# Performance work log

Hardware: AMD Instinct MI355X
Metric: run time of the kernel (lower is better)

Reference implementation:

```python
import jax, jax.numpy as jnp
import numpy as np

B, H, KVH, D = 64, 32, 8, 128     # batch, q heads, kv heads, head dim
BS, MB = 16, 128                  # paged-cache block size, max blocks per seq
NB = B * MB                       # total cache blocks (8192)
L = MB * BS                       # max kv length per sequence (2048)
SCALE = 0.08838834764831845       # 1/sqrt(head_dim)


def setup_inputs() -> dict:
    key = jax.random.key(0)
    ks = jax.random.split(key, 6)
    q = jax.random.normal(ks[0], (B, H * D), jnp.float32)
    k = jax.random.normal(ks[1], (B, KVH * D), jnp.float32)
    v = jax.random.normal(ks[2], (B, KVH * D), jnp.float32)
    k_cache = jax.random.normal(ks[3], (NB, BS, KVH, D), jnp.float32)
    v_cache = jax.random.normal(ks[4], (NB, BS, KVH, D), jnp.float32)
    # each sequence owns MB disjoint contiguous blocks
    block_tables = jnp.arange(B * MB, dtype=jnp.int32).reshape(B, MB)
    context_lens = jax.random.randint(ks[5], (B,), 0, L - 1, dtype=jnp.int32)
    return dict(q=q, k=k, v=v, k_cache=k_cache, v_cache=v_cache,
                block_tables=block_tables, context_lens=context_lens)


def reference(q, k, v, k_cache, v_cache, block_tables, context_lens):
    G = H // KVH  # GQA group size
    qh = q.reshape(B, KVH, G, D)
    kh = k.reshape(B, KVH, D)
    vh = v.reshape(B, KVH, D)
    # store new token's KV at its paged slot (position = context_len)
    slots = block_tables[jnp.arange(B), context_lens // BS] * BS + context_lens % BS
    kc = k_cache.reshape(NB * BS, KVH, D).at[slots].set(kh)
    vc = v_cache.reshape(NB * BS, KVH, D).at[slots].set(vh)
    # gather paged KV per sequence via block tables -> [B, L, KVH, D]
    keys = kc.reshape(NB, BS, KVH, D)[block_tables].reshape(B, L, KVH, D)
    vals = vc.reshape(NB, BS, KVH, D)[block_tables].reshape(B, L, KVH, D)
    # GQA attention: each kv head serves G query heads
    scores = jnp.einsum('bkgd,blkd->bkgl', qh, keys) * SCALE
    valid = jnp.arange(L)[None, :] <= context_lens[:, None]  # [B, L], inclusive of new token
    scores = jnp.where(valid[:, None, None, :], scores, jnp.float32(-jnp.inf))
    w = jax.nn.softmax(scores, axis=-1)
    out = jnp.einsum('bkgl,blkd->bkgd', w, vals)
    return out.reshape(B, H * D)
```

## Files before the change

kernel.cpp:

```cpp
#include <hip/hip_runtime.h>
#include <hip/hip_fp16.h>

#define BATCH 64
#define NHEADS 32
#define KVH 8
#define HDIM 128
#define GQA 4
#define BLKSZ 16
#define MAXBLK 128
#define MAXLEN 2048
#define SCALE 0.08838834764831845f

#define CHUNK 64
#define MAXITEMS 2048
#define REC_BYTES 320u
#define SLOT_BYTES 4096u
#define WS_REC_FLOATS ((size_t)MAXITEMS * KVH * GQA * (REC_BYTES / 4))
#define WS_FLOATS (WS_REC_FLOATS + 80)

typedef unsigned int uint;
typedef float f32x4 __attribute__((ext_vector_type(4)));

struct KVBuf { float4 k0, k1, v0, v1; };

template<int CTRL>
__device__ __forceinline__ float dppAdd(float x) {
    int y = __builtin_amdgcn_update_dpp(0, __float_as_int(x), CTRL, 0xf, 0xf, false);
    return x + __int_as_float(y);
}

__device__ __forceinline__ float halfSum(float v, bool upper) {
    v = dppAdd<0x111>(v);
    v = dppAdd<0x112>(v);
    v = dppAdd<0x114>(v);
    v = dppAdd<0x118>(v);
    v = dppAdd<0x142>(v);
    const float lo = __int_as_float(__builtin_amdgcn_readlane(__float_as_int(v), 31));
    const float hi = __int_as_float(__builtin_amdgcn_readlane(__float_as_int(v), 63));
    return upper ? hi : lo;
}

__global__ void pa_scan(const int* __restrict__ context_lens, uint* __restrict__ offs) {
    const int t = threadIdx.x;
    int cnt = (t < BATCH) ? (context_lens[t] + 1 + CHUNK - 1) / CHUNK : 0;
    #pragma unroll
    for (int o = 1; o < 64; o <<= 1) {
        const int v = __shfl_up(cnt, o, 64);
        if (t >= o) cnt += v;
    }
    offs[t + 1] = (uint)cnt;
    if (t == 0) offs[0] = 0u;
}

__global__ __launch_bounds__(256, 4) void pa_partial(
    const float* __restrict__ q,
    const float* __restrict__ knew,
    const float* __restrict__ vnew,
    const float* __restrict__ k_cache,
    const float* __restrict__ v_cache,
    const int*   __restrict__ block_tables,
    const int*   __restrict__ context_lens,
    float* __restrict__ ws,
    const uint*  __restrict__ offs)
{
    const uint item = blockIdx.x;
    if (item >= offs[BATCH]) return;

    int lo = 0, hi = BATCH;
    while (lo + 1 < hi) {
        const int mid = (lo + hi) >> 1;
        if (item >= offs[mid]) lo = mid; else hi = mid;
    }
    const int b    = lo;
    const int part = (int)(item - offs[b]);

    const int cl = context_lens[b];
    const int n  = cl + 1;
    const int p0 = part * CHUNK;
    const int pend = min(p0 + CHUNK, n);

    const int tid  = threadIdx.x;
    const int kvh  = tid >> 5;
    const int lane = tid & 31;
    const bool upperHalf = (tid & 32) != 0;
    const uint laneByte = ((uint)kvh << 9) + ((uint)lane << 4);

    float4 qf[GQA];
    #pragma unroll
    for (int g = 0; g < GQA; ++g) {
        float4 t = *reinterpret_cast<const float4*>(
            &q[(size_t)b * (NHEADS * HDIM) + (size_t)(kvh * GQA + g) * HDIM + lane * 4]);
        t.x *= SCALE; t.y *= SCALE; t.z *= SCALE; t.w *= SCALE;
        qf[g] = t;
    }

    float  s[GQA];
    float4 acc[GQA];
    #pragma unroll
    for (int g = 0; g < GQA; ++g) {
        s[g] = 0.f;
        acc[g] = make_float4(0.f, 0.f, 0.f, 0.f);
    }

    const char* kc8 = reinterpret_cast<const char*>(k_cache);
    const char* vc8 = reinterpret_cast<const char*>(v_cache);

    if (p0 + CHUNK <= cl) {
        int blkv[4];
        #pragma unroll
        for (int c = 0; c < 4; ++c)
            blkv[c] = block_tables[b * MAXBLK + (p0 >> 4) + c];

        KVBuf bufA, bufB;

#define ISSUE(P, i)                                                              \
        {                                                                        \
            const uint u0 = ((uint)blkv[(2*(i)) >> 4] * BLKSZ + ((2*(i)) & 15)) * SLOT_BYTES + laneByte; \
            const uint u1 = ((uint)blkv[(2*(i)+1) >> 4] * BLKSZ + ((2*(i)+1) & 15)) * SLOT_BYTES + laneByte; \
            buf##P.k0 = *reinterpret_cast<const float4*>(kc8 + u0);              \
            buf##P.k1 = *reinterpret_cast<const float4*>(kc8 + u1);              \
            buf##P.v0 = *reinterpret_cast<const float4*>(vc8 + u0);              \
            buf##P.v1 = *reinterpret_cast<const float4*>(vc8 + u1);              \
        }

#define CONSUME(P)                                                               \
        {                                                                        \
            float sc0[GQA], sc1[GQA];                                            \
            _Pragma("unroll")                                                    \
            for (int g = 0; g < GQA; ++g) {                                      \
                sc0[g] = buf##P.k0.x * qf[g].x + buf##P.k0.y * qf[g].y           \
                       + buf##P.k0.z * qf[g].z + buf##P.k0.w * qf[g].w;          \
                sc1[g] = buf##P.k1.x * qf[g].x + buf##P.k1.y * qf[g].y           \
                       + buf##P.k1.z * qf[g].z + buf##P.k1.w * qf[g].w;          \
            }                                                                    \
            _Pragma("unroll")                                                    \
            for (int g = 0; g < GQA; ++g) {                                      \
                sc0[g] = halfSum(sc0[g], upperHalf);                             \
                sc1[g] = halfSum(sc1[g], upperHalf);                             \
            }                                                                    \
            _Pragma("unroll")                                                    \
            for (int g = 0; g < GQA; ++g) {                                      \
                const float e0 = __expf(sc0[g]);                                 \
                const float e1 = __expf(sc1[g]);                                 \
                s[g] += e0 + e1;                                                 \
                acc[g].x += e0 * buf##P.v0.x + e1 * buf##P.v1.x;                 \
                acc[g].y += e0 * buf##P.v0.y + e1 * buf##P.v1.y;                 \
                acc[g].z += e0 * buf##P.v0.z + e1 * buf##P.v1.z;                 \
                acc[g].w += e0 * buf##P.v0.w + e1 * buf##P.v1.w;                 \
            }                                                                    \
        }

        ISSUE(A, 0);
        #pragma unroll
        for (int i = 0; i < 31; ++i) {
            if (i & 1) { ISSUE(A, i + 1); CONSUME(B); }
            else       { ISSUE(B, i + 1); CONSUME(A); }
        }
        CONSUME(B);
#undef ISSUE
#undef CONSUME
    } else {
        const int* bt = &block_tables[b * MAXBLK];
        const float* knrow = &knew[((size_t)b * KVH + kvh) * HDIM + lane * 4];
        const float* vnrow = &vnew[((size_t)b * KVH + kvh) * HDIM + lane * 4];

        for (int t0 = p0; t0 < pend; t0 += 4) {
            bool valid[4];
            const float* kp[4];
            const float* vp[4];
            #pragma unroll
            for (int j = 0; j < 4; ++j) {
                const int l = t0 + j;
                valid[j] = (l < pend);
                if (!valid[j] || l == cl) {
                    kp[j] = knrow; vp[j] = vnrow;
                } else {
                    const int blk = bt[l >> 4];
                    const uint u  = ((uint)blk * BLKSZ + (l & 15)) * SLOT_BYTES + laneByte;
                    kp[j] = reinterpret_cast<const float*>(kc8 + u);
                    vp[j] = reinterpret_cast<const float*>(vc8 + u);
                }
            }

            float4 kf[4], vf[4];
            #pragma unroll
            for (int j = 0; j < 4; ++j) kf[j] = *reinterpret_cast<const float4*>(kp[j]);
            #pragma unroll
            for (int j = 0; j < 4; ++j) vf[j] = *reinterpret_cast<const float4*>(vp[j]);

            float sc[4][GQA];
            #pragma unroll
            for (int j = 0; j < 4; ++j)
                #pragma unroll
                for (int g = 0; g < GQA; ++g)
                    sc[j][g] = kf[j].x * qf[g].x + kf[j].y * qf[g].y
                             + kf[j].z * qf[g].z + kf[j].w * qf[g].w;

            #pragma unroll
            for (int off = 16; off > 0; off >>= 1)
                #pragma unroll
                for (int j = 0; j < 4; ++j)
                    #pragma unroll
                    for (int g = 0; g < GQA; ++g)
                        sc[j][g] += __shfl_xor(sc[j][g], off, 32);

            #pragma unroll
            for (int g = 0; g < GQA; ++g) {
                float p[4];
                #pragma unroll
                for (int j = 0; j < 4; ++j)
                    p[j] = valid[j] ? __expf(sc[j][g]) : 0.f;
                s[g] += (p[0] + p[1]) + (p[2] + p[3]);
                acc[g].x += p[0] * vf[0].x + p[1] * vf[1].x + p[2] * vf[2].x + p[3] * vf[3].x;
                acc[g].y += p[0] * vf[0].y + p[1] * vf[1].y + p[2] * vf[2].y + p[3] * vf[3].y;
                acc[g].z += p[0] * vf[0].z + p[1] * vf[1].z + p[2] * vf[2].z + p[3] * vf[3].z;
                acc[g].w += p[0] * vf[0].w + p[1] * vf[1].w + p[2] * vf[2].w + p[3] * vf[3].w;
            }
        }
    }

    char* rec = reinterpret_cast<char*>(ws)
              + (size_t)(item * KVH + kvh) * GQA * REC_BYTES;
    #pragma unroll
    for (int g = 0; g < GQA; ++g) {
        __half2 h01 = __floats2half2_rn(acc[g].x, acc[g].y);
        __half2 h23 = __floats2half2_rn(acc[g].z, acc[g].w);
        uint2 pk;
        pk.x = *reinterpret_cast<uint*>(&h01);
        pk.y = *reinterpret_cast<uint*>(&h23);
        *reinterpret_cast<uint2*>(rec + (size_t)g * REC_BYTES + lane * 8) = pk;
    }
    if (lane == 0) {
        #pragma unroll
        for (int g = 0; g < GQA; ++g)
            *reinterpret_cast<float*>(rec + (size_t)g * REC_BYTES + 256) = s[g];
    }
}

__global__ __launch_bounds__(128) void pa_reduce(
    const float* __restrict__ ws,
    const uint*  __restrict__ offs,
    float* __restrict__ out)
{
    const int bh   = blockIdx.x;
    const int b    = bh >> 3;
    const int kvh  = bh & 7;
    const int t    = threadIdx.x;
    const int g    = t >> 5;
    const int lane = t & 31;

    const uint i0   = offs[b];
    const int  pcnt = (int)(offs[b + 1] - i0);

    const char* base = reinterpret_cast<const char*>(ws)
                     + ((size_t)(i0 * KVH + kvh) * GQA + g) * REC_BYTES;
    const size_t pstride = (size_t)KVH * GQA * REC_BYTES;

    f32x4 O0 = {0,0,0,0}, O1 = {0,0,0,0}, O2 = {0,0,0,0}, O3 = {0,0,0,0};
    float S0 = 0.f, S1 = 0.f, S2 = 0.f, S3 = 0.f;

#define ACCREC(Ov, Sv, rp)                                                       \
    {                                                                            \
        const uint2 pk = *reinterpret_cast<const uint2*>((rp) + lane * 8);       \
        const float2 f01 = __half22float2(*reinterpret_cast<const __half2*>(&pk.x)); \
        const float2 f23 = __half22float2(*reinterpret_cast<const __half2*>(&pk.y)); \
        Ov.x += f01.x; Ov.y += f01.y; Ov.z += f23.x; Ov.w += f23.y;              \
        Sv += *reinterpret_cast<const float*>((rp) + 256);                       \
    }

    int p = 0;
    for (; p + 4 <= pcnt; p += 4) {
        const char* r0 = base + (size_t)(p + 0) * pstride;
        const char* r1 = base + (size_t)(p + 1) * pstride;
        const char* r2 = base + (size_t)(p + 2) * pstride;
        const char* r3 = base + (size_t)(p + 3) * pstride;
        ACCREC(O0, S0, r0);
        ACCREC(O1, S1, r1);
        ACCREC(O2, S2, r2);
        ACCREC(O3, S3, r3);
    }
    for (; p < pcnt; ++p) {
        const char* r = base + (size_t)p * pstride;
        ACCREC(O0, S0, r);
    }
#undef ACCREC

    const f32x4 O = (O0 + O1) + (O2 + O3);
    const float S = (S0 + S1) + (S2 + S3);
    const float inv = 1.0f / S;

    float* op = &out[(size_t)b * (NHEADS * HDIM) + (size_t)(kvh * GQA + g) * HDIM + lane * 4];
    *reinterpret_cast<f32x4*>(op) = O * inv;
}

__global__ __launch_bounds__(256) void paged_attn_decode(
    const float* __restrict__ q,
    const float* __restrict__ knew,
    const float* __restrict__ vnew,
    const float* __restrict__ k_cache,
    const float* __restrict__ v_cache,
    const int*   __restrict__ block_tables,
    const int*   __restrict__ context_lens,
    float* __restrict__ out)
{
    const int bh   = blockIdx.x;
    const int b    = bh / KVH;
    const int kvh  = bh % KVH;
    const int tid  = threadIdx.x;
    const int hw   = tid >> 5;
    const int lane = tid & 31;

    const int cl = context_lens[b];
    const int n  = cl + 1;

    float4 qf[GQA];
    #pragma unroll
    for (int g = 0; g < GQA; ++g) {
        float4 t = *reinterpret_cast<const float4*>(
            &q[(size_t)b * (NHEADS * HDIM) + (size_t)(kvh * GQA + g) * HDIM + lane * 4]);
        t.x *= SCALE; t.y *= SCALE; t.z *= SCALE; t.w *= SCALE;
        qf[g] = t;
    }

    float  s[GQA];
    float4 acc[GQA];
    #pragma unroll
    for (int g = 0; g < GQA; ++g) { s[g] = 0.f; acc[g] = make_float4(0.f,0.f,0.f,0.f); }

    const int* bt = &block_tables[b * MAXBLK];

    for (int l = hw; l < n; l += 8) {
        const float4* krow;
        const float4* vrow;
        if (l == cl) {
            krow = reinterpret_cast<const float4*>(&knew[(size_t)(b * KVH + kvh) * HDIM]);
            vrow = reinterpret_cast<const float4*>(&vnew[(size_t)(b * KVH + kvh) * HDIM]);
        } else {
            const int    blk = bt[l >> 4];
            const size_t off = (((size_t)blk * BLKSZ + (l & 15)) * KVH + kvh) * HDIM;
            krow = reinterpret_cast<const float4*>(&k_cache[off]);
            vrow = reinterpret_cast<const float4*>(&v_cache[off]);
        }
        const float4 kf = krow[lane];
        const float4 vf = vrow[lane];

        float sc[GQA];
        #pragma unroll
        for (int g = 0; g < GQA; ++g)
            sc[g] = kf.x * qf[g].x + kf.y * qf[g].y + kf.z * qf[g].z + kf.w * qf[g].w;

        #pragma unroll
        for (int off = 16; off > 0; off >>= 1)
            #pragma unroll
            for (int g = 0; g < GQA; ++g)
                sc[g] += __shfl_xor(sc[g], off, 32);

        #pragma unroll
        for (int g = 0; g < GQA; ++g) {
            const float p = __expf(sc[g]);
            s[g] += p;
            acc[g].x += p * vf.x; acc[g].y += p * vf.y;
            acc[g].z += p * vf.z; acc[g].w += p * vf.w;
        }
    }

    __shared__ float lds_s[8][GQA];
    __shared__ float lds_acc[8][GQA][HDIM];

    #pragma unroll
    for (int g = 0; g < GQA; ++g)
        *reinterpret_cast<float4*>(&lds_acc[hw][g][lane * 4]) = acc[g];
    if (lane == 0) {
        #pragma unroll
        for (int g = 0; g < GQA; ++g) lds_s[hw][g] = s[g];
    }
    __syncthreads();

    for (int i = tid; i < GQA * HDIM; i += 256) {
        const int g = i >> 7;
        const int d = i & 127;
        float S = 0.f, O = 0.f;
        #pragma unroll
        for (int h = 0; h < 8; ++h) { S += lds_s[h][g]; O += lds_acc[h][g][d]; }
        out[(size_t)b * (NHEADS * HDIM) + (size_t)(kvh * GQA + g) * HDIM + d] = O / S;
    }
}

extern "C" void kernel_launch(void* const* d_in, const int* in_sizes, int n_in,
                              void* d_out, int out_size, void* d_ws, size_t ws_size,
                              hipStream_t stream) {
    const float* q      = (const float*)d_in[0];
    const float* k      = (const float*)d_in[1];
    const float* v      = (const float*)d_in[2];
    const float* kc     = (const float*)d_in[3];
    const float* vc     = (const float*)d_in[4];
    const int*   bt     = (const int*)d_in[5];
    const int*   clens  = (const int*)d_in[6];
    float*       out    = (float*)d_out;

    if (ws_size >= WS_FLOATS * sizeof(float)) {
        float* ws   = (float*)d_ws;
        uint*  offs = (uint*)(ws + WS_REC_FLOATS);
        pa_scan<<<dim3(1), dim3(64), 0, stream>>>(clens, offs);
        pa_partial<<<dim3(MAXITEMS), dim3(256), 0, stream>>>(
            q, k, v, kc, vc, bt, clens, ws, offs);
        pa_reduce<<<dim3(BATCH * KVH), dim3(128), 0, stream>>>(ws, offs, out);
    } else {
        paged_attn_decode<<<dim3(BATCH * KVH), dim3(256), 0, stream>>>(
            q, k, v, kc, vc, bt, clens, out);
    }
}
```

Measured before the change: 118.3 us.

## Fuse scan, partial and reduce kernels into one with last-block reduction

Every workgroup now computes the chunk prefix offsets itself in shared memory, which removes the separate scan kernel. The last workgroup to finish for a sequence, detected with an atomic counter, performs that sequence's cross-chunk reduction, which removes the separate reduce kernel. Three launches become one memset plus one kernel. The trade-offs are a redundant scan in every block, threadfences and atomics, and a serial tail where a single block reduces all 8 heads of a sequence.

```diff
diff --git a/kernel.cpp b/kernel.cpp
--- a/kernel.cpp
+++ b/kernel.cpp
@@ -16,7 +16,7 @@
 #define REC_BYTES 320u
 #define SLOT_BYTES 4096u
 #define WS_REC_FLOATS ((size_t)MAXITEMS * KVH * GQA * (REC_BYTES / 4))
-#define WS_FLOATS (WS_REC_FLOATS + 80)
+#define WS_FLOATS (WS_REC_FLOATS + 64)
 
 typedef unsigned int uint;
 typedef float f32x4 __attribute__((ext_vector_type(4)));
@@ -40,19 +40,7 @@
     return upper ? hi : lo;
 }
 
-__global__ void pa_scan(const int* __restrict__ context_lens, uint* __restrict__ offs) {
-    const int t = threadIdx.x;
-    int cnt = (t < BATCH) ? (context_lens[t] + 1 + CHUNK - 1) / CHUNK : 0;
-    #pragma unroll
-    for (int o = 1; o < 64; o <<= 1) {
-        const int v = __shfl_up(cnt, o, 64);
-        if (t >= o) cnt += v;
-    }
-    offs[t + 1] = (uint)cnt;
-    if (t == 0) offs[0] = 0u;
-}
-
-__global__ __launch_bounds__(256, 4) void pa_partial(
+__global__ __launch_bounds__(256, 4) void pa_fused(
     const float* __restrict__ q,
     const float* __restrict__ knew,
     const float* __restrict__ vnew,
@@ -61,25 +49,44 @@
     const int*   __restrict__ block_tables,
     const int*   __restrict__ context_lens,
     float* __restrict__ ws,
-    const uint*  __restrict__ offs)
+    uint*  __restrict__ ctr,
+    float* __restrict__ out)
 {
+    __shared__ uint s_offs[BATCH + 1];
+    __shared__ int  s_last;
+
+    const int tid = threadIdx.x;
+
+    if (tid < 64) {
+        int cnt = (tid < BATCH) ? (context_lens[tid] + 1 + CHUNK - 1) / CHUNK : 0;
+        #pragma unroll
+        for (int o = 1; o < 64; o <<= 1) {
+            const int v = __shfl_up(cnt, o, 64);
+            if (tid >= o) cnt += v;
+        }
+        s_offs[tid + 1] = (uint)cnt;
+        if (tid == 0) s_offs[0] = 0u;
+    }
+    __syncthreads();
+
     const uint item = blockIdx.x;
-    if (item >= offs[BATCH]) return;
+    if (item >= s_offs[BATCH]) return;
 
     int lo = 0, hi = BATCH;
     while (lo + 1 < hi) {
         const int mid = (lo + hi) >> 1;
-        if (item >= offs[mid]) lo = mid; else hi = mid;
+        if (item >= s_offs[mid]) lo = mid; else hi = mid;
     }
     const int b    = lo;
-    const int part = (int)(item - offs[b]);
+    const int part = (int)(item - s_offs[b]);
+    const uint i0  = s_offs[b];
+    const int pcnt = (int)(s_offs[b + 1] - i0);
 
     const int cl = context_lens[b];
     const int n  = cl + 1;
     const int p0 = part * CHUNK;
     const int pend = min(p0 + CHUNK, n);
 
-    const int tid  = threadIdx.x;
     const int kvh  = tid >> 5;
     const int lane = tid & 31;
     const bool upperHalf = (tid & 32) != 0;
@@ -219,78 +226,72 @@
         }
     }
 
-    char* rec = reinterpret_cast<char*>(ws)
-              + (size_t)(item * KVH + kvh) * GQA * REC_BYTES;
-    #pragma unroll
-    for (int g = 0; g < GQA; ++g) {
-        __half2 h01 = __floats2half2_rn(acc[g].x, acc[g].y);
-        __half2 h23 = __floats2half2_rn(acc[g].z, acc[g].w);
-        uint2 pk;
-        pk.x = *reinterpret_cast<uint*>(&h01);
-        pk.y = *reinterpret_cast<uint*>(&h23);
-        *reinterpret_cast<uint2*>(rec + (size_t)g * REC_BYTES + lane * 8) = pk;
-    }
-    if (lane == 0) {
-        #pragma unroll
-        for (int g = 0; g < GQA; ++g)
-            *reinterpret_cast<float*>(rec + (size_t)g * REC_BYTES + 256) = s[g];
-    }
-}
-
-__global__ __launch_bounds__(128) void pa_reduce(
-    const float* __restrict__ ws,
-    const uint*  __restrict__ offs,
-    float* __restrict__ out)
-{
-    const int bh   = blockIdx.x;
-    const int b    = bh >> 3;
-    const int kvh  = bh & 7;
-    const int t    = threadIdx.x;
-    const int g    = t >> 5;
-    const int lane = t & 31;
-
-    const uint i0   = offs[b];
-    const int  pcnt = (int)(offs[b + 1] - i0);
-
-    const char* base = reinterpret_cast<const char*>(ws)
-                     + ((size_t)(i0 * KVH + kvh) * GQA + g) * REC_BYTES;
+    char* ws8 = reinterpret_cast<char*>(ws);
+    {
+        char* rec = ws8 + (size_t)(item * KVH + kvh) * GQA * REC_BYTES;
+        #pragma unroll
+        for (int g = 0; g < GQA; ++g) {
+            __half2 h01 = __floats2half2_rn(acc[g].x, acc[g].y);
+            __half2 h23 = __floats2half2_rn(acc[g].z, acc[g].w);
+            uint2 pk;
+            pk.x = *reinterpret_cast<uint*>(&h01);
+            pk.y = *reinterpret_cast<uint*>(&h23);
+            *reinterpret_cast<uint2*>(rec + (size_t)g * REC_BYTES + lane * 8) = pk;
+        }
+        if (lane == 0) {
+            #pragma unroll
+            for (int g = 0; g < GQA; ++g)
+                *reinterpret_cast<float*>(rec + (size_t)g * REC_BYTES + 256) = s[g];
+        }
+    }
+
+    __threadfence();
+    __syncthreads();
+    if (tid == 0)
+        s_last = (atomicAdd(&ctr[b], 1u) == (uint)(pcnt - 1));
+    __syncthreads();
+    if (!s_last) return;
+    __threadfence();
+
     const size_t pstride = (size_t)KVH * GQA * REC_BYTES;
-
-    f32x4 O0 = {0,0,0,0}, O1 = {0,0,0,0}, O2 = {0,0,0,0}, O3 = {0,0,0,0};
-    float S0 = 0.f, S1 = 0.f, S2 = 0.f, S3 = 0.f;
+    for (int unit = tid; unit < KVH * GQA * 32; unit += 256) {
+        const int rkvh  = unit >> 7;
+        const int rg    = (unit >> 5) & 3;
+        const int rlane = unit & 31;
+
+        const char* base = ws8 + ((size_t)(i0 * KVH + rkvh) * GQA + rg) * REC_BYTES;
+
+        f32x4 O0 = {0,0,0,0}, O1 = {0,0,0,0}, O2 = {0,0,0,0}, O3 = {0,0,0,0};
+        float S0 = 0.f, S1 = 0.f, S2 = 0.f, S3 = 0.f;
 
 #define ACCREC(Ov, Sv, rp)                                                       \
-    {                                                                            \
-        const uint2 pk = *reinterpret_cast<const uint2*>((rp) + lane * 8);       \
-        const float2 f01 = __half22float2(*reinterpret_cast<const __half2*>(&pk.x)); \
-        const float2 f23 = __half22float2(*reinterpret_cast<const __half2*>(&pk.y)); \
-        Ov.x += f01.x; Ov.y += f01.y; Ov.z += f23.x; Ov.w += f23.y;              \
-        Sv += *reinterpret_cast<const float*>((rp) + 256);                       \
-    }
-
-    int p = 0;
-    for (; p + 4 <= pcnt; p += 4) {
-        const char* r0 = base + (size_t)(p + 0) * pstride;
-        const char* r1 = base + (size_t)(p + 1) * pstride;
-        const char* r2 = base + (size_t)(p + 2) * pstride;
-        const char* r3 = base + (size_t)(p + 3) * pstride;
-        ACCREC(O0, S0, r0);
-        ACCREC(O1, S1, r1);
-        ACCREC(O2, S2, r2);
-        ACCREC(O3, S3, r3);
-    }
-    for (; p < pcnt; ++p) {
-        const char* r = base + (size_t)p * pstride;
-        ACCREC(O0, S0, r);
-    }
+        {                                                                        \
+            const uint2 pk = *reinterpret_cast<const uint2*>((rp) + rlane * 8);  \
+            const float2 f01 = __half22float2(*reinterpret_cast<const __half2*>(&pk.x)); \
+            const float2 f23 = __half22float2(*reinterpret_cast<const __half2*>(&pk.y)); \
+            Ov.x += f01.x; Ov.y += f01.y; Ov.z += f23.x; Ov.w += f23.y;          \
+            Sv += *reinterpret_cast<const float*>((rp) + 256);                   \
+        }
+
+        int p = 0;
+        for (; p + 4 <= pcnt; p += 4) {
+            ACCREC(O0, S0, base + (size_t)(p + 0) * pstride);
+            ACCREC(O1, S1, base + (size_t)(p + 1) * pstride);
+            ACCREC(O2, S2, base + (size_t)(p + 2) * pstride);
+            ACCREC(O3, S3, base + (size_t)(p + 3) * pstride);
+        }
+        for (; p < pcnt; ++p)
+            ACCREC(O0, S0, base + (size_t)p * pstride);
 #undef ACCREC
 
-    const f32x4 O = (O0 + O1) + (O2 + O3);
-    const float S = (S0 + S1) + (S2 + S3);
-    const float inv = 1.0f / S;
-
-    float* op = &out[(size_t)b * (NHEADS * HDIM) + (size_t)(kvh * GQA + g) * HDIM + lane * 4];
-    *reinterpret_cast<f32x4*>(op) = O * inv;
+        const f32x4 O = (O0 + O1) + (O2 + O3);
+        const float S = (S0 + S1) + (S2 + S3);
+        const float inv = 1.0f / S;
+
+        float* op = &out[(size_t)b * (NHEADS * HDIM)
+                         + (size_t)(rkvh * GQA + rg) * HDIM + rlane * 4];
+        *reinterpret_cast<f32x4*>(op) = O * inv;
+    }
 }
 
 __global__ __launch_bounds__(256) void paged_attn_decode(
@@ -399,12 +400,11 @@
     float*       out    = (float*)d_out;
 
     if (ws_size >= WS_FLOATS * sizeof(float)) {
-        float* ws   = (float*)d_ws;
-        uint*  offs = (uint*)(ws + WS_REC_FLOATS);
-        pa_scan<<<dim3(1), dim3(64), 0, stream>>>(clens, offs);
-        pa_partial<<<dim3(MAXITEMS), dim3(256), 0, stream>>>(
-            q, k, v, kc, vc, bt, clens, ws, offs);
-        pa_reduce<<<dim3(BATCH * KVH), dim3(128), 0, stream>>>(ws, offs, out);
+        float* ws  = (float*)d_ws;
+        uint*  ctr = (uint*)(ws + WS_REC_FLOATS);
+        hipMemsetAsync(ctr, 0, BATCH * sizeof(uint), stream);
+        pa_fused<<<dim3(MAXITEMS), dim3(256), 0, stream>>>(
+            q, k, v, kc, vc, bt, clens, ws, ctr, out);
     } else {
         paged_attn_decode<<<dim3(BATCH * KVH), dim3(256), 0, stream>>>(
             q, k, v, kc, vc, bt, clens, out);
```

After: 337.4 us. 2.85x slower.
